# Optimization experiments

Hardware: AMD Instinct MI355X
Metric: run time of the kernel (lower is better)

The kernel has to match this reference:

```python
import jax, jax.numpy as jnp
import numpy as np

B, D, N, H, DOUT = 2048, 64, 16384, 4, 256
ALPHA = 1.0
BETA = 1.0
EPS = 1e-12


def setup_inputs() -> dict:
    key = jax.random.key(0)
    k1, k2, k3, k4 = jax.random.split(key, 4)
    x = jax.random.normal(k1, (B, D), dtype=jnp.float32)
    # lecun_normal-like init for anchors and combine weights
    R = jax.random.normal(k2, (N, D), dtype=jnp.float32) * (1.0 / np.sqrt(D))
    q_raw = jnp.ones((H, N), dtype=jnp.float32)  # nn.initializers.ones
    # perturb q a bit so the power-law reweighting is non-trivial
    q_raw = q_raw + 0.1 * jax.random.uniform(k3, (H, N), dtype=jnp.float32)
    W = jax.random.normal(k4, (H, N, DOUT), dtype=jnp.float32) * (1.0 / np.sqrt(N))
    return {"x": x, "R": R, "q_raw": q_raw, "W": W}


def reference(x, R, q_raw, W):
    # SMD (euclidean): squared distance to anchors, shared across heads
    x2 = jnp.sum(x * x, axis=-1, keepdims=True)            # (B, 1)
    cross = -2.0 * (x @ R.T)                                # (B, N)
    R2 = jnp.sum(R * R, axis=-1)                            # (N,)
    dist2 = jnp.maximum(x2 + cross + R2, 0.0)               # (B, N)
    dist2_h = jnp.broadcast_to(dist2[:, None, :], (x.shape[0], H, N))  # (B, H, N)
    # per-head beta scale + relu safety
    beta = jnp.full((H,), BETA, dtype=jnp.float32).reshape(1, H, 1)
    dist2_h = jax.nn.relu(dist2_h * beta)
    logits = -dist2_h
    # power-law reweighted softmax
    z = logits - jnp.max(logits, axis=-1, keepdims=True)
    w = jnp.exp(z)
    q = jax.nn.relu(q_raw) + EPS                             # (H, N)
    w = w * q ** (-ALPHA)
    p = w / (jnp.sum(w, axis=-1, keepdims=True) + EPS)       # (B, H, N)
    # per-head weighted combine (W is (H, N, d) as in the source)
    y = jnp.einsum('bhn,hnd->bhd', p, W)                     # (B, H, d)
    return y.astype(jnp.float32)
```

## Files before the change

### kernel.cpp

```cpp
#include <hip/hip_runtime.h>
#include <cstdint>
#include <cstddef>

#define B_DIM 2048
#define D_DIM 64
#define N_DIM 16384
#define H_DIM 4
#define DOUT_DIM 256
#define NOUT (H_DIM*DOUT_DIM)

typedef __bf16 bf16;
typedef __bf16 bf16x4 __attribute__((ext_vector_type(4)));
typedef __bf16 bf16x8 __attribute__((ext_vector_type(8)));
typedef float f32x4 __attribute__((ext_vector_type(4)));

#define LOG2E 1.44269504088896340736f

#define PREP_RBLK 4096
#define PREP_XBLK 512
__global__ void k_prep(const float* __restrict__ x, const float* __restrict__ R,
                       bf16* __restrict__ xh, bf16* __restrict__ xl,
                       bf16* __restrict__ Rh, bf16* __restrict__ Rl,
                       float* __restrict__ r2) {
    int blk = blockIdx.x, t = threadIdx.x;
    if (blk < PREP_RBLK) {
        int lane = t & 63, wave = t >> 6;
        int row = blk * 4 + wave;
        float v = R[row * 64 + lane];
        bf16 h = (bf16)v;
        Rh[row * 64 + lane] = h;
        Rl[row * 64 + lane] = (bf16)(v - (float)h);
        float s = v * v;
        #pragma unroll
        for (int off = 32; off > 0; off >>= 1) s += __shfl_xor(s, off, 64);
        if (lane == 0) r2[row] = s;
    } else {
        int i = (blk - PREP_RBLK) * 256 + t;
        float f = 2.0f * x[i];
        bf16 h = (bf16)f;
        xh[i] = h;
        xl[i] = (bf16)(f - (float)h);
    }
}

__global__ void k_build_V(const float* __restrict__ W, const float* __restrict__ q_raw,
                          bf16* __restrict__ Vt) {
    __shared__ float tile[64][33];
    __shared__ float qprow[64];
    int h = blockIdx.z, d0 = blockIdx.y * 32, n0 = blockIdx.x * 64;
    int t = threadIdx.x;
    int tj = t & 31, ti = t >> 5;
    if (t < 64)
        qprow[t] = 1.0f / (fmaxf(q_raw[h * N_DIM + n0 + t], 0.0f) + 1e-12f);
    #pragma unroll
    for (int ii = 0; ii < 8; ++ii) {
        int i = ti + ii * 8;
        tile[i][tj] = W[((size_t)(h * N_DIM) + (n0 + i)) * DOUT_DIM + d0 + tj];
    }
    __syncthreads();
    int d = t >> 3, nq = t & 7;
    bf16x8 ov;
    #pragma unroll
    for (int j = 0; j < 8; ++j) {
        int n = nq * 8 + j;
        ov[j] = (bf16)(tile[n][d] * qprow[n]);
    }
    *(bf16x8*)(Vt + (size_t)(h * DOUT_DIM + d0 + d) * N_DIM + n0 + nq * 8) = ov;
}

__launch_bounds__(256)
__global__ void k_scores(const bf16* __restrict__ xh, const bf16* __restrict__ xl,
                         const bf16* __restrict__ Rh, const bf16* __restrict__ Rl,
                         const float* __restrict__ r2, const float* __restrict__ q_raw,
                         bf16* __restrict__ e, float* __restrict__ Spart) {
    __shared__ bf16 eT[128][136];
    __shared__ float qp[4][128];
    int n0 = blockIdx.x * 128;
    int row0 = blockIdx.y * 128;
    int t = threadIdx.x;
    int lane = t & 63, w = t >> 6;
    int wr = w >> 1, wc = w & 1;
    #pragma unroll
    for (int rr = 0; rr < 2; ++rr) {
        int ii = t + rr * 256;
        qp[ii >> 7][ii & 127] =
            1.0f / (fmaxf(q_raw[(ii >> 7) * N_DIM + n0 + (ii & 127)], 0.0f) + 1e-12f);
    }
    int l15 = lane & 15, l4 = lane >> 4;
    f32x4 acc[4][4] = {};
    #pragma unroll
    for (int kk = 0; kk < 2; ++kk) {
        bf16x8 bxh[4], bxl[4];
        #pragma unroll
        for (int ni = 0; ni < 4; ++ni) {
            int b = row0 + wc * 64 + ni * 16 + l15;
            size_t off = (size_t)b * 64 + kk * 32 + l4 * 8;
            bxh[ni] = *(const bf16x8*)(xh + off);
            bxl[ni] = *(const bf16x8*)(xl + off);
        }
        #pragma unroll
        for (int mi = 0; mi < 4; ++mi) {
            int n = n0 + wr * 64 + mi * 16 + l15;
            size_t off = (size_t)n * 64 + kk * 32 + l4 * 8;
            bf16x8 arh = *(const bf16x8*)(Rh + off);
            bf16x8 arl = *(const bf16x8*)(Rl + off);
            #pragma unroll
            for (int ni = 0; ni < 4; ++ni) {
                acc[mi][ni] = __builtin_amdgcn_mfma_f32_16x16x32_bf16(arh, bxh[ni], acc[mi][ni], 0, 0, 0);
                acc[mi][ni] = __builtin_amdgcn_mfma_f32_16x16x32_bf16(arh, bxl[ni], acc[mi][ni], 0, 0, 0);
                acc[mi][ni] = __builtin_amdgcn_mfma_f32_16x16x32_bf16(arl, bxh[ni], acc[mi][ni], 0, 0, 0);
            }
        }
    }
    #pragma unroll
    for (int mi = 0; mi < 4; ++mi) {
        int keyb = wr * 64 + mi * 16 + l4 * 4;
        f32x4 r2v = *(const f32x4*)(r2 + n0 + keyb);
        #pragma unroll
        for (int ni = 0; ni < 4; ++ni) {
            int bloc = wc * 64 + ni * 16 + l15;
            bf16x4 ev;
            #pragma unroll
            for (int j = 0; j < 4; ++j) {
                float s = acc[mi][ni][j] - r2v[j];
                ev[j] = (bf16)exp2f(s * LOG2E);
            }
            *(bf16x4*)(&eT[bloc][keyb]) = ev;
        }
    }
    __syncthreads();
    {
        int bloc = t >> 1, half = t & 1;
        int b = row0 + bloc;
        bf16x8 chunk[8];
        #pragma unroll
        for (int i = 0; i < 8; ++i)
            chunk[i] = *(const bf16x8*)(&eT[bloc][half * 64 + i * 8]);
        bf16x8* gp = (bf16x8*)(e + (size_t)b * N_DIM + n0 + half * 64);
        #pragma unroll
        for (int i = 0; i < 8; ++i) gp[i] = chunk[i];
        float s0 = 0, s1 = 0, s2 = 0, s3 = 0;
        #pragma unroll
        for (int i = 0; i < 8; ++i) {
            #pragma unroll
            for (int jj = 0; jj < 8; ++jj) {
                int nl = half * 64 + i * 8 + jj;
                float ef = (float)chunk[i][jj];
                s0 += ef * qp[0][nl]; s1 += ef * qp[1][nl];
                s2 += ef * qp[2][nl]; s3 += ef * qp[3][nl];
            }
        }
        s0 += __shfl_xor(s0, 1, 64);
        s1 += __shfl_xor(s1, 1, 64);
        s2 += __shfl_xor(s2, 1, 64);
        s3 += __shfl_xor(s3, 1, 64);
        if (half == 0) {
            f32x4 sv = {s0, s1, s2, s3};
            *(f32x4*)(Spart + ((size_t)blockIdx.x * B_DIM + b) * 4) = sv;
        }
    }
}

__global__ void k_sreduce(const float* __restrict__ Spart, float* __restrict__ Sinv) {
    int i = blockIdx.x * 256 + threadIdx.x;
    float s = 0.f;
    #pragma unroll 8
    for (int kt = 0; kt < N_DIM / 128; ++kt) s += Spart[(size_t)kt * (B_DIM * 4) + i];
    Sinv[i] = 1.0f / (s + 1e-12f);
}

__launch_bounds__(256)
__global__ void k_gemm(const bf16* __restrict__ e, const bf16* __restrict__ Vt,
                       float* __restrict__ parts, int kiters) {
    __shared__ bf16 As[128 * 64];
    __shared__ bf16 Bs[128 * 64];
    int t = threadIdx.x;
    int lane = t & 63, w = t >> 6;
    int wr = w >> 1, wc = w & 1;
    int nwg = gridDim.x * gridDim.y * gridDim.z;
    int cpx = nwg >> 3;
    int flat = blockIdx.x + 8 * (blockIdx.y + 16 * blockIdx.z);
    int orig = (flat & 7) * cpx + (flat >> 3);
    int bx = orig & 7;
    int by = (orig >> 3) & 15;
    int bz = orig >> 7;
    int brow = by * 128;
    int bcol = bx * 128;
    int kbase = bz * kiters * 64;
    int l15 = lane & 15, l4 = lane >> 4;
    int srcRow = lane >> 3;
    int srcColB = (lane & 7) * 16;
    f32x4 acc[4][4] = {};
    for (int kt = 0; kt < kiters; ++kt) {
        int k0 = kbase + kt * 64;
        #pragma unroll
        for (int j = 0; j < 4; ++j) {
            int chunk = j * 4 + w;
            int row = chunk * 8 + srcRow;
            const char* gA = (const char*)e + ((size_t)(brow + row) * N_DIM + k0) * 2 + srcColB;
            __builtin_amdgcn_global_load_lds((const __attribute__((address_space(1))) void*)gA,
                (__attribute__((address_space(3))) void*)((char*)As + chunk * 1024), 16, 0, 0);
            const char* gB = (const char*)Vt + ((size_t)(bcol + row) * N_DIM + k0) * 2 + srcColB;
            __builtin_amdgcn_global_load_lds((const __attribute__((address_space(1))) void*)gB,
                (__attribute__((address_space(3))) void*)((char*)Bs + chunk * 1024), 16, 0, 0);
        }
        __syncthreads();
        #pragma unroll
        for (int kk = 0; kk < 2; ++kk) {
            bf16x8 bfr[4];
            #pragma unroll
            for (int ni = 0; ni < 4; ++ni)
                bfr[ni] = *(const bf16x8*)(Bs + (wc * 64 + ni * 16 + l15) * 64 + kk * 32 + l4 * 8);
            #pragma unroll
            for (int mi = 0; mi < 4; ++mi) {
                bf16x8 afr = *(const bf16x8*)(As + (wr * 64 + mi * 16 + l15) * 64 + kk * 32 + l4 * 8);
                #pragma unroll
                for (int ni = 0; ni < 4; ++ni)
                    acc[mi][ni] = __builtin_amdgcn_mfma_f32_16x16x32_bf16(afr, bfr[ni], acc[mi][ni], 0, 0, 0);
            }
        }
        __syncthreads();
    }
    float* P = parts + (size_t)bz * ((size_t)B_DIM * NOUT);
    #pragma unroll
    for (int mi = 0; mi < 4; ++mi) {
        #pragma unroll
        for (int j = 0; j < 4; ++j) {
            int r = brow + wr * 64 + mi * 16 + l4 * 4 + j;
            #pragma unroll
            for (int ni = 0; ni < 4; ++ni) {
                int c = bcol + wc * 64 + ni * 16 + l15;
                P[(size_t)r * NOUT + c] = acc[mi][ni][j];
            }
        }
    }
}

__global__ void k_final(const float* __restrict__ parts, const float* __restrict__ Sinv,
                        float* __restrict__ out, int nks) {
    int i4 = blockIdx.x * 256 + threadIdx.x;
    size_t base = (size_t)i4 * 4;
    f32x4 s = {0.f, 0.f, 0.f, 0.f};
    for (int k = 0; k < nks; ++k)
        s += *(const f32x4*)(parts + (size_t)k * ((size_t)B_DIM * NOUT) + base);
    int b = i4 >> 8;
    int c = (i4 << 2) & 1023;
    float inv = Sinv[b * 4 + (c >> 8)];
    *(f32x4*)(out + base) = s * inv;
}

extern "C" void kernel_launch(void* const* d_in, const int* in_sizes, int n_in,
                              void* d_out, int out_size, void* d_ws, size_t ws_size,
                              hipStream_t stream) {
    const float* x     = (const float*)d_in[0];
    const float* R     = (const float*)d_in[1];
    const float* q_raw = (const float*)d_in[2];
    const float* W     = (const float*)d_in[3];
    float* out = (float*)d_out;

    char* ws = (char*)d_ws;
    size_t off = 0;
    auto alloc = [&](size_t bytes) {
        void* p = ws + off;
        off += (bytes + 255) & ~(size_t)255;
        return p;
    };
    bf16*  Vt    = (bf16*) alloc((size_t)NOUT * N_DIM * 2);
    bf16*  eM    = (bf16*) alloc((size_t)B_DIM * N_DIM * 2);
    bf16*  xh    = (bf16*) alloc((size_t)B_DIM * D_DIM * 2);
    bf16*  xl    = (bf16*) alloc((size_t)B_DIM * D_DIM * 2);
    bf16*  Rh    = (bf16*) alloc((size_t)N_DIM * D_DIM * 2);
    bf16*  Rl    = (bf16*) alloc((size_t)N_DIM * D_DIM * 2);
    float* r2    = (float*)alloc((size_t)N_DIM * 4);
    float* Spart = (float*)alloc((size_t)(N_DIM / 128) * B_DIM * 4 * 4);
    float* Sinv  = (float*)alloc((size_t)B_DIM * H_DIM * 4);
    (void)n_in; (void)in_sizes;

    const size_t PART_BYTES = (size_t)B_DIM * NOUT * 4;
    int ksplit = (ws_size >= off + 8 * PART_BYTES) ? 8
               : (ws_size >= off + 4 * PART_BYTES) ? 4 : 2;
    float* parts = (float*)alloc((size_t)ksplit * PART_BYTES);
    int kiters = N_DIM / (64 * ksplit);

    k_prep<<<dim3(PREP_RBLK + PREP_XBLK), 256, 0, stream>>>(x, R, xh, xl, Rh, Rl, r2);
    k_build_V<<<dim3(N_DIM / 64, DOUT_DIM / 32, H_DIM), 256, 0, stream>>>(W, q_raw, Vt);
    k_scores<<<dim3(N_DIM / 128, B_DIM / 128), 256, 0, stream>>>(xh, xl, Rh, Rl, r2, q_raw, eM, Spart);
    k_sreduce<<<dim3(B_DIM * H_DIM / 256), 256, 0, stream>>>(Spart, Sinv);
    k_gemm<<<dim3(NOUT / 128, B_DIM / 128, ksplit), 256, 0, stream>>>(eM, Vt, parts, kiters);
    k_final<<<dim3(B_DIM * NOUT / 4 / 256), 256, 0, stream>>>(parts, Sinv, out, ksplit);
}
```

Measured before the change: 292.0 us.

## Add 4-stage LDS pipeline with XOR swizzle to bf16 GEMM kernel

Changes the k_gemm main loop from one synchronous load-then-compute step to a 4-deep ring of LDS buffers. Tiles are prefetched three iterations ahead with global_load_lds, and progress is tracked with manual vmcnt waits and raw s_barrier, so memory latency overlaps MFMA work. It also XOR-swizzles the LDS column layout to reduce bank conflicts on fragment reads, and raises wave priority during compute. LDS use grows fourfold to 128KB per block, which may cut occupancy. The loop also assumes kiters >= 3.

```diff
diff --git a/kernel.cpp b/kernel.cpp
--- a/kernel.cpp
+++ b/kernel.cpp
@@ -172,8 +172,7 @@
 __launch_bounds__(256)
 __global__ void k_gemm(const bf16* __restrict__ e, const bf16* __restrict__ Vt,
                        float* __restrict__ parts, int kiters) {
-    __shared__ bf16 As[128 * 64];
-    __shared__ bf16 Bs[128 * 64];
+    __shared__ bf16 AB[4][2][8192];
     int t = threadIdx.x;
     int lane = t & 63, w = t >> 6;
     int wr = w >> 1, wc = w & 1;
@@ -188,39 +187,89 @@
     int bcol = bx * 128;
     int kbase = bz * kiters * 64;
     int l15 = lane & 15, l4 = lane >> 4;
-    int srcRow = lane >> 3;
-    int srcColB = (lane & 7) * 16;
+    const char* eC  = (const char*)e;
+    const char* VtC = (const char*)Vt;
+    int scolswz = (((lane & 7) ^ (lane >> 3)) << 4);
+    int srow = lane >> 3;
+
+#define STAGE(bi, tile) do {                                                              \
+    size_t acol = (size_t)(kbase + (tile) * 64) * 2 + scolswz;                            \
+    _Pragma("unroll")                                                                     \
+    for (int j_ = 0; j_ < 4; ++j_) {                                                      \
+        int chunk_ = j_ * 4 + w;                                                          \
+        int row_ = chunk_ * 8 + srow;                                                     \
+        __builtin_amdgcn_global_load_lds(                                                 \
+            (const __attribute__((address_space(1))) void*)(eC + (size_t)(brow + row_) * (N_DIM*2) + acol), \
+            (__attribute__((address_space(3))) void*)((char*)&AB[bi][0][0] + chunk_ * 1024), 16, 0, 0); \
+        __builtin_amdgcn_global_load_lds(                                                 \
+            (const __attribute__((address_space(1))) void*)(VtC + (size_t)(bcol + row_) * (N_DIM*2) + acol), \
+            (__attribute__((address_space(3))) void*)((char*)&AB[bi][1][0] + chunk_ * 1024), 16, 0, 0); \
+    }                                                                                     \
+} while (0)
+
+#define COMPUTE(bi) do {                                                                  \
+    const bf16* As_ = &AB[bi][0][0];                                                      \
+    const bf16* Bs_ = &AB[bi][1][0];                                                      \
+    _Pragma("unroll")                                                                     \
+    for (int kk = 0; kk < 2; ++kk) {                                                      \
+        bf16x8 bfr[4], afr[4];                                                            \
+        _Pragma("unroll")                                                                 \
+        for (int ni = 0; ni < 4; ++ni) {                                                  \
+            int row_ = wc * 64 + ni * 16 + l15;                                           \
+            int col_ = (kk * 32 + l4 * 8) ^ ((row_ & 7) << 3);                            \
+            bfr[ni] = *(const bf16x8*)(Bs_ + row_ * 64 + col_);                           \
+        }                                                                                 \
+        _Pragma("unroll")                                                                 \
+        for (int mi = 0; mi < 4; ++mi) {                                                  \
+            int row_ = wr * 64 + mi * 16 + l15;                                           \
+            int col_ = (kk * 32 + l4 * 8) ^ ((row_ & 7) << 3);                            \
+            afr[mi] = *(const bf16x8*)(As_ + row_ * 64 + col_);                           \
+        }                                                                                 \
+        _Pragma("unroll")                                                                 \
+        for (int mi = 0; mi < 4; ++mi)                                                    \
+            _Pragma("unroll")                                                             \
+            for (int ni = 0; ni < 4; ++ni)                                                \
+                acc[mi][ni] = __builtin_amdgcn_mfma_f32_16x16x32_bf16(afr[mi], bfr[ni], acc[mi][ni], 0, 0, 0); \
+    }                                                                                     \
+} while (0)
+
     f32x4 acc[4][4] = {};
-    for (int kt = 0; kt < kiters; ++kt) {
-        int k0 = kbase + kt * 64;
-        #pragma unroll
-        for (int j = 0; j < 4; ++j) {
-            int chunk = j * 4 + w;
-            int row = chunk * 8 + srcRow;
-            const char* gA = (const char*)e + ((size_t)(brow + row) * N_DIM + k0) * 2 + srcColB;
-            __builtin_amdgcn_global_load_lds((const __attribute__((address_space(1))) void*)gA,
-                (__attribute__((address_space(3))) void*)((char*)As + chunk * 1024), 16, 0, 0);
-            const char* gB = (const char*)Vt + ((size_t)(bcol + row) * N_DIM + k0) * 2 + srcColB;
-            __builtin_amdgcn_global_load_lds((const __attribute__((address_space(1))) void*)gB,
-                (__attribute__((address_space(3))) void*)((char*)Bs + chunk * 1024), 16, 0, 0);
-        }
-        __syncthreads();
-        #pragma unroll
-        for (int kk = 0; kk < 2; ++kk) {
-            bf16x8 bfr[4];
-            #pragma unroll
-            for (int ni = 0; ni < 4; ++ni)
-                bfr[ni] = *(const bf16x8*)(Bs + (wc * 64 + ni * 16 + l15) * 64 + kk * 32 + l4 * 8);
-            #pragma unroll
-            for (int mi = 0; mi < 4; ++mi) {
-                bf16x8 afr = *(const bf16x8*)(As + (wr * 64 + mi * 16 + l15) * 64 + kk * 32 + l4 * 8);
-                #pragma unroll
-                for (int ni = 0; ni < 4; ++ni)
-                    acc[mi][ni] = __builtin_amdgcn_mfma_f32_16x16x32_bf16(afr, bfr[ni], acc[mi][ni], 0, 0, 0);
-            }
-        }
-        __syncthreads();
-    }
+    STAGE(0, 0);
+    STAGE(1, 1);
+    STAGE(2, 2);
+    for (int kt = 0; kt <= kiters - 4; ++kt) {
+        int bi = kt & 3;
+        STAGE((kt + 3) & 3, kt + 3);
+        asm volatile("s_waitcnt vmcnt(24)" ::: "memory");
+        __builtin_amdgcn_sched_barrier(0);
+        asm volatile("s_barrier" ::: "memory");
+        __builtin_amdgcn_s_setprio(1);
+        COMPUTE(bi);
+        __builtin_amdgcn_s_setprio(0);
+        asm volatile("s_barrier" ::: "memory");
+    }
+    {
+        asm volatile("s_waitcnt vmcnt(16)" ::: "memory");
+        __builtin_amdgcn_sched_barrier(0);
+        asm volatile("s_barrier" ::: "memory");
+        COMPUTE((kiters - 3) & 3);
+        asm volatile("s_barrier" ::: "memory");
+    }
+    {
+        asm volatile("s_waitcnt vmcnt(8)" ::: "memory");
+        __builtin_amdgcn_sched_barrier(0);
+        asm volatile("s_barrier" ::: "memory");
+        COMPUTE((kiters - 2) & 3);
+        asm volatile("s_barrier" ::: "memory");
+    }
+    {
+        asm volatile("s_waitcnt vmcnt(0)" ::: "memory");
+        __builtin_amdgcn_sched_barrier(0);
+        asm volatile("s_barrier" ::: "memory");
+        COMPUTE((kiters - 1) & 3);
+    }
+#undef STAGE
+#undef COMPUTE
     float* P = parts + (size_t)bz * ((size_t)B_DIM * NOUT);
     #pragma unroll
     for (int mi = 0; mi < 4; ++mi) {
```

Result: faster. 284.4 us (-2.6%).
